# Performance work log

Hardware: AMD Instinct MI355X
Metric: run time of the kernel (lower is better)

The kernel has to match this reference:

```python
import jax, jax.numpy as jnp
import numpy as np

EPS = 1e-5

def layer_norm(x, g, b):
    m = jnp.mean(x, axis=-1, keepdims=True)
    v = jnp.mean((x - m) ** 2, axis=-1, keepdims=True)
    return (x - m) / jnp.sqrt(v + EPS) * g + b

def setup_inputs() -> dict:
    key = jax.random.key(0)
    ks = jax.random.split(key, 20)
    B, N, Fin, Fout, H, Fe = 8, 1024, 128, 128, 8, 16
    s = 0.02
    inp = {
        'x': jax.random.normal(ks[0], (B, N, Fin), jnp.float32),
        'adj': jax.random.randint(ks[1], (B, N, N), 0, 2, dtype=jnp.int32),
        'edge_attr': jax.random.normal(ks[2], (B, N, N, Fe), jnp.float32),
        'ln1_g': jnp.ones((Fin,), jnp.float32),
        'ln1_b': jnp.zeros((Fin,), jnp.float32),
        'Wp': s * jax.random.normal(ks[3], (Fout, Fin), jnp.float32),
        'bp': jnp.zeros((Fout,), jnp.float32),
        'eln_g': jnp.ones((Fe,), jnp.float32),
        'eln_b': jnp.zeros((Fe,), jnp.float32),
        'We1': s * jax.random.normal(ks[4], (2 * Fe, Fe), jnp.float32),
        'be1': jnp.zeros((2 * Fe,), jnp.float32),
        'We2': s * jax.random.normal(ks[5], (H, 2 * Fe), jnp.float32),
        'be2': jnp.zeros((H,), jnp.float32),
        'Wq': s * jax.random.normal(ks[6], (Fout, Fout), jnp.float32),
        'Wk': s * jax.random.normal(ks[7], (Fout, Fout), jnp.float32),
        'Wv': s * jax.random.normal(ks[8], (Fout, Fout), jnp.float32),
        'W1': s * jax.random.normal(ks[9], (2 * Fout, Fout), jnp.float32),
        'b1': jnp.zeros((2 * Fout,), jnp.float32),
        'W2': s * jax.random.normal(ks[10], (Fout, 2 * Fout), jnp.float32),
        'b2': jnp.zeros((Fout,), jnp.float32),
        'ln2_g': jnp.ones((Fout,), jnp.float32),
        'ln2_b': jnp.zeros((Fout,), jnp.float32),
    }
    return inp

def reference(x, adj, edge_attr, ln1_g, ln1_b, Wp, bp, eln_g, eln_b,
              We1, be1, We2, be2, Wq, Wk, Wv, W1, b1, W2, b2, ln2_g, ln2_b):
    B, N, _ = x.shape
    H = We2.shape[0]
    Fout = Wp.shape[0]
    Dh = Fout // H
    x_norm = layer_norm(x, ln1_g, ln1_b)
    x_proj = x_norm @ Wp.T + bp                       # [B,N,Fout]
    Q = (x_proj @ Wq.T).reshape(B, N, H, Dh).transpose(0, 2, 1, 3)  # [B,H,N,Dh]
    K = (x_proj @ Wk.T).reshape(B, N, H, Dh).transpose(0, 2, 1, 3)
    V = (x_proj @ Wv.T).reshape(B, N, H, Dh).transpose(0, 2, 1, 3)
    scores = jnp.einsum('bhnd,bhmd->bhnm', Q, K) / jnp.sqrt(jnp.float32(Dh))
    # edge bias MLP
    e = layer_norm(edge_attr, eln_g, eln_b)           # [B,N,N,Fe]
    e = jax.nn.relu(e @ We1.T + be1)
    edge_bias = (e @ We2.T + be2)                     # [B,N,N,H]
    scores = scores + edge_bias.transpose(0, 3, 1, 2)  # [B,H,N,N]
    scores = jnp.where(scores >= 0, scores, 0.2 * scores)  # LeakyReLU(0.2)
    mask = adj[:, None, :, :] != 0                    # [B,1,N,N]
    scores = jnp.where(mask, scores, jnp.float32(-1e9))
    probs = jax.nn.softmax(scores, axis=-1)
    context = jnp.einsum('bhnm,bhmd->bhnd', probs, V)  # [B,H,N,Dh]
    context = context.transpose(0, 2, 1, 3).reshape(B, N, Fout)
    h_attn = x_proj + context
    h = layer_norm(h_attn, ln2_g, ln2_b)
    h = jax.nn.relu(h @ W1.T + b1) @ W2.T + b2
    return h_attn + h
```

## Files before the change

kernel.cpp:

```cpp
#include <hip/hip_runtime.h>

#define LOG2E 1.44269504088896f

typedef __attribute__((ext_vector_type(8))) short bf8v;
typedef __attribute__((ext_vector_type(16))) float f16v;

union B8 { bf8v v; short s[8]; unsigned u[4]; uint2 d[2]; uint4 q; };
union F16 { f16v v; float f[16]; };

__device__ __forceinline__ unsigned short f2bf(float f) {
    union { float f; unsigned u; } c; c.f = f;
    unsigned r = c.u + 0x7FFFu + ((c.u >> 16) & 1u);
    return (unsigned short)(r >> 16);
}
__device__ __forceinline__ unsigned pk2(float a, float b) {
    return (unsigned)f2bf(a) | ((unsigned)f2bf(b) << 16);
}
__device__ __forceinline__ int rowpat(int reg, int half) {
    return (reg & 3) + 8 * (reg >> 2) + 4 * half;
}

__global__ __launch_bounds__(64) void ln_kernel(const float* __restrict__ x,
                                                const float* __restrict__ g,
                                                const float* __restrict__ b,
                                                float* __restrict__ y) {
    int row = blockIdx.x;
    int lane = threadIdx.x;
    const float* xr = x + (size_t)row * 128;
    float2 v = *(const float2*)(xr + lane * 2);
    float s = v.x + v.y;
    float sq = v.x * v.x + v.y * v.y;
    #pragma unroll
    for (int o = 32; o > 0; o >>= 1) { s += __shfl_xor(s, o); sq += __shfl_xor(sq, o); }
    float m = s * (1.f / 128.f);
    float var = sq * (1.f / 128.f) - m * m;
    float r = rsqrtf(fmaxf(var, 0.f) + 1e-5f);
    float2 gg = *(const float2*)(g + lane * 2);
    float2 bb = *(const float2*)(b + lane * 2);
    float2 o2;
    o2.x = (v.x - m) * r * gg.x + bb.x;
    o2.y = (v.y - m) * r * gg.y + bb.y;
    *(float2*)(y + (size_t)row * 128 + lane * 2) = o2;
}

__global__ __launch_bounds__(256) void gemm_kernel(const float* __restrict__ A,
                                                   const float* __restrict__ W,
                                                   const float* __restrict__ bias,
                                                   float* __restrict__ out,
                                                   const float* __restrict__ res,
                                                   int K, int ldo, int mode) {
    int t = threadIdx.x, w = t >> 6, lane = t & 63;
    int lm = lane & 31, half = lane >> 5;
    int row0 = blockIdx.x * 128 + w * 32;
    int col0 = blockIdx.y * 32;
    const float* ap = A + (size_t)(row0 + lm) * K + half * 8;
    const float* wp = W + (size_t)(col0 + lm) * K + half * 8;
    F16 acc;
    #pragma unroll
    for (int i = 0; i < 16; i++) acc.f[i] = 0.f;
    for (int k0 = 0; k0 < K; k0 += 16) {
        float4 a0 = *(const float4*)(ap + k0);
        float4 a1 = *(const float4*)(ap + k0 + 4);
        float4 w0 = *(const float4*)(wp + k0);
        float4 w1 = *(const float4*)(wp + k0 + 4);
        B8 af, wf;
        af.u[0] = pk2(a0.x, a0.y); af.u[1] = pk2(a0.z, a0.w);
        af.u[2] = pk2(a1.x, a1.y); af.u[3] = pk2(a1.z, a1.w);
        wf.u[0] = pk2(w0.x, w0.y); wf.u[1] = pk2(w0.z, w0.w);
        wf.u[2] = pk2(w1.x, w1.y); wf.u[3] = pk2(w1.z, w1.w);
        acc.v = __builtin_amdgcn_mfma_f32_32x32x16_bf16(af.v, wf.v, acc.v, 0, 0, 0);
    }
    float bv = bias ? bias[col0 + lm] : 0.f;
    int col = col0 + lm;
    #pragma unroll
    for (int reg = 0; reg < 16; reg++) {
        int row = row0 + rowpat(reg, half);
        float v = acc.f[reg] + bv;
        if (mode == 1) v = fmaxf(v, 0.f);
        if (mode == 2) v += res[(size_t)row * ldo + col];
        out[(size_t)row * ldo + col] = v;
    }
}

__global__ __launch_bounds__(512) void attn_kernel(
    const float* __restrict__ Qm, const float* __restrict__ Km, const float* __restrict__ Vm,
    const float* __restrict__ xp, const float* __restrict__ ea, const int* __restrict__ adj,
    const float* __restrict__ We1, const float* __restrict__ be1,
    const float* __restrict__ We2, const float* __restrict__ be2,
    const float* __restrict__ eg, const float* __restrict__ eb,
    float* __restrict__ ha) {
    __shared__ short smK[32][132];
    __shared__ short smVt[128][36];
    __shared__ float smBias[8480];
    __shared__ short smH1[8][1280];

    int b = blockIdx.x, i0 = blockIdx.y * 32;
    int t = threadIdx.x, w = t >> 6;
    int lane = t & 63, lm = lane & 31, half = lane >> 5;

    B8 qf, w1f, w2a, w2b;
    {
        const float* qp = Qm + (size_t)(b * 1024 + i0 + lm) * 128 + w * 16 + half * 8;
        float4 q0 = *(const float4*)qp, q1 = *(const float4*)(qp + 4);
        qf.u[0] = pk2(q0.x * 0.25f, q0.y * 0.25f); qf.u[1] = pk2(q0.z * 0.25f, q0.w * 0.25f);
        qf.u[2] = pk2(q1.x * 0.25f, q1.y * 0.25f); qf.u[3] = pk2(q1.z * 0.25f, q1.w * 0.25f);
    }
    {
        const float* wp = We1 + lm * 16 + half * 8;
        #pragma unroll
        for (int j = 0; j < 8; j++) w1f.s[j] = (short)f2bf(wp[j] * eg[half * 8 + j]);
    }
    {
        int hs = lm & 7;
        #pragma unroll
        for (int j = 0; j < 8; j++) {
            w2a.s[j] = (short)f2bf(We2[hs * 32 + half * 8 + j]);
            w2b.s[j] = (short)f2bf(We2[hs * 32 + 16 + half * 8 + j]);
        }
    }
    float c1r[16];
    #pragma unroll
    for (int reg = 0; reg < 16; reg++) {
        int ch = rowpat(reg, half);
        float sacc = be1[ch];
        const float* wr = We1 + ch * 16;
        #pragma unroll
        for (int j = 0; j < 16; j++) sacc += wr[j] * eb[j];
        c1r[reg] = sacc;
    }
    float be2r[4];
    #pragma unroll
    for (int r = 0; r < 4; r++) be2r[r] = be2[r + 4 * half];

    F16 ou;
    #pragma unroll
    for (int i = 0; i < 16; i++) ou.f[i] = 0.f;
    float mrun = -3.0e38f, lrun = 0.f;

    #pragma unroll 1
    for (int nj = 0; nj < 32; nj++) {
        int j0 = nj * 32;
        __syncthreads();
        {
            int rr = t >> 4, fc = (t & 15) * 8;
            const float* kp = Km + (size_t)(b * 1024 + j0 + rr) * 128 + fc;
            float4 k0 = *(const float4*)kp, k1 = *(const float4*)(kp + 4);
            uint2 p0; p0.x = pk2(k0.x, k0.y); p0.y = pk2(k0.z, k0.w);
            uint2 p1; p1.x = pk2(k1.x, k1.y); p1.y = pk2(k1.z, k1.w);
            *(uint2*)&smK[rr][fc] = p0;
            *(uint2*)&smK[rr][fc + 4] = p1;
            const float* vp = Vm + (size_t)(b * 1024 + j0 + rr) * 128 + fc;
            float4 v0 = *(const float4*)vp, v1 = *(const float4*)(vp + 4);
            smVt[fc + 0][rr] = (short)f2bf(v0.x); smVt[fc + 1][rr] = (short)f2bf(v0.y);
            smVt[fc + 2][rr] = (short)f2bf(v0.z); smVt[fc + 3][rr] = (short)f2bf(v0.w);
            smVt[fc + 4][rr] = (short)f2bf(v1.x); smVt[fc + 5][rr] = (short)f2bf(v1.y);
            smVt[fc + 6][rr] = (short)f2bf(v1.z); smVt[fc + 7][rr] = (short)f2bf(v1.w);
        }
        short* hrow = &smH1[w][lm * 40];
        for (int s4 = 0; s4 < 4; s4++) {
            int ti = w * 4 + s4;
            const float* ep = ea + ((size_t)(b * 1024 + i0 + ti) * 1024 + j0 + lm) * 16 + half * 8;
            float4 e0 = *(const float4*)ep, e1 = *(const float4*)(ep + 4);
            float sum = e0.x + e0.y + e0.z + e0.w + e1.x + e1.y + e1.z + e1.w;
            float sq = e0.x * e0.x + e0.y * e0.y + e0.z * e0.z + e0.w * e0.w
                     + e1.x * e1.x + e1.y * e1.y + e1.z * e1.z + e1.w * e1.w;
            sum += __shfl_xor(sum, 32); sq += __shfl_xor(sq, 32);
            float mn = sum * 0.0625f;
            float rs = rsqrtf(fmaxf(sq * 0.0625f - mn * mn, 0.f) + 1e-5f);
            float mr = mn * rs;
            B8 ef;
            ef.u[0] = pk2(e0.x * rs - mr, e0.y * rs - mr);
            ef.u[1] = pk2(e0.z * rs - mr, e0.w * rs - mr);
            ef.u[2] = pk2(e1.x * rs - mr, e1.y * rs - mr);
            ef.u[3] = pk2(e1.z * rs - mr, e1.w * rs - mr);
            F16 z;
            #pragma unroll
            for (int i = 0; i < 16; i++) z.f[i] = 0.f;
            F16 h1; h1.v = __builtin_amdgcn_mfma_f32_32x32x16_bf16(w1f.v, ef.v, z.v, 0, 0, 0);
            #pragma unroll
            for (int pr = 0; pr < 8; pr++) {
                int r0 = 2 * pr;
                int ch0 = rowpat(r0, half);
                float a0 = fmaxf(h1.f[r0] + c1r[r0], 0.f);
                float a1 = fmaxf(h1.f[r0 + 1] + c1r[r0 + 1], 0.f);
                *(unsigned*)(hrow + ch0) = pk2(a0, a1);
            }
            B8 hba, hbb;
            hba.q = *(const uint4*)(hrow + half * 8);
            hbb.q = *(const uint4*)(hrow + 16 + half * 8);
            F16 b2; b2.v = __builtin_amdgcn_mfma_f32_32x32x16_bf16(w2a.v, hba.v, z.v, 0, 0, 0);
            b2.v = __builtin_amdgcn_mfma_f32_32x32x16_bf16(w2b.v, hbb.v, b2.v, 0, 0, 0);
            int aj = adj[(size_t)(b * 1024 + i0 + ti) * 1024 + j0 + lm];
            #pragma unroll
            for (int reg = 0; reg < 4; reg++) {
                float bvv = aj ? (b2.f[reg] + be2r[reg]) : -1.0e9f;
                smBias[lm * 265 + (reg + 4 * half) * 33 + ti] = bvv;
            }
        }
        __syncthreads();
        F16 sc;
        #pragma unroll
        for (int reg = 0; reg < 16; reg++) {
            int tj = rowpat(reg, half);
            sc.f[reg] = smBias[tj * 265 + w * 33 + lm];
        }
        B8 kf;
        {
            const short* kp2 = &smK[lm][w * 16 + half * 8];
            kf.d[0] = *(const uint2*)kp2; kf.d[1] = *(const uint2*)(kp2 + 4);
        }
        F16 s; s.v = __builtin_amdgcn_mfma_f32_32x32x16_bf16(kf.v, qf.v, sc.v, 0, 0, 0);
        float mx = -3.0e38f;
        #pragma unroll
        for (int reg = 0; reg < 16; reg++) {
            float vv = s.f[reg];
            vv = fmaxf(vv, 0.2f * vv);
            s.f[reg] = vv;
            mx = fmaxf(mx, vv);
        }
        mx = fmaxf(mx, __shfl_xor(mx, 32));
        float mnew = fmaxf(mrun, mx);
        float al = exp2f((mrun - mnew) * LOG2E);
        float psum = 0.f;
        #pragma unroll
        for (int reg = 0; reg < 16; reg++) {
            float p = exp2f((s.f[reg] - mnew) * LOG2E);
            s.f[reg] = p; psum += p;
        }
        lrun = lrun * al + psum; mrun = mnew;
        unsigned q0 = pk2(s.f[0], s.f[1]), q0b = pk2(s.f[2], s.f[3]);
        unsigned q1 = pk2(s.f[4], s.f[5]), q1b = pk2(s.f[6], s.f[7]);
        unsigned q2 = pk2(s.f[8], s.f[9]), q2b = pk2(s.f[10], s.f[11]);
        unsigned q3 = pk2(s.f[12], s.f[13]), q3b = pk2(s.f[14], s.f[15]);
        unsigned x0 = __shfl_xor((int)q0, 32), x0b = __shfl_xor((int)q0b, 32);
        unsigned x1 = __shfl_xor((int)q1, 32), x1b = __shfl_xor((int)q1b, 32);
        unsigned x2 = __shfl_xor((int)q2, 32), x2b = __shfl_xor((int)q2b, 32);
        unsigned x3 = __shfl_xor((int)q3, 32), x3b = __shfl_xor((int)q3b, 32);
        B8 pfa, pfb;
        pfa.u[0] = half ? x1 : q0;  pfa.u[1] = half ? x1b : q0b;
        pfa.u[2] = half ? q1 : x0;  pfa.u[3] = half ? q1b : x0b;
        pfb.u[0] = half ? x3 : q2;  pfb.u[1] = half ? x3b : q2b;
        pfb.u[2] = half ? q3 : x2;  pfb.u[3] = half ? q3b : x2b;
        #pragma unroll
        for (int reg = 0; reg < 16; reg++) {
            float av = __shfl(al, rowpat(reg, half));
            ou.f[reg] *= av;
        }
        int dcol = lm & 15;
        const short* vp2 = &smVt[w * 16 + dcol][half * 8];
        B8 vfa, vfb;
        vfa.d[0] = *(const uint2*)vp2;        vfa.d[1] = *(const uint2*)(vp2 + 4);
        vfb.d[0] = *(const uint2*)(vp2 + 16); vfb.d[1] = *(const uint2*)(vp2 + 20);
        ou.v = __builtin_amdgcn_mfma_f32_32x32x16_bf16(pfa.v, vfa.v, ou.v, 0, 0, 0);
        ou.v = __builtin_amdgcn_mfma_f32_32x32x16_bf16(pfb.v, vfb.v, ou.v, 0, 0, 0);
    }
    float ltot = lrun + __shfl_xor(lrun, 32);
    float linv = 1.f / ltot;
    int dcol = lm & 15;
    #pragma unroll
    for (int reg = 0; reg < 16; reg++) {
        int row = rowpat(reg, half);
        float lv = __shfl(linv, row);
        if (lm < 16) {
            size_t gi = (size_t)(b * 1024 + i0 + row) * 128 + w * 16 + dcol;
            ha[gi] = ou.f[reg] * lv + xp[gi];
        }
    }
}

extern "C" void kernel_launch(void* const* d_in, const int* in_sizes, int n_in,
                              void* d_out, int out_size, void* d_ws, size_t ws_size,
                              hipStream_t stream) {
    (void)in_sizes; (void)n_in; (void)out_size; (void)ws_size;
    const float* x    = (const float*)d_in[0];
    const int*   adj  = (const int*)d_in[1];
    const float* ea   = (const float*)d_in[2];
    const float* ln1g = (const float*)d_in[3];
    const float* ln1b = (const float*)d_in[4];
    const float* Wp   = (const float*)d_in[5];
    const float* bp   = (const float*)d_in[6];
    const float* eg   = (const float*)d_in[7];
    const float* eb   = (const float*)d_in[8];
    const float* We1  = (const float*)d_in[9];
    const float* be1  = (const float*)d_in[10];
    const float* We2  = (const float*)d_in[11];
    const float* be2  = (const float*)d_in[12];
    const float* Wq   = (const float*)d_in[13];
    const float* Wk   = (const float*)d_in[14];
    const float* Wv   = (const float*)d_in[15];
    const float* W1   = (const float*)d_in[16];
    const float* b1   = (const float*)d_in[17];
    const float* W2   = (const float*)d_in[18];
    const float* b2   = (const float*)d_in[19];
    const float* ln2g = (const float*)d_in[20];
    const float* ln2b = (const float*)d_in[21];
    float* out = (float*)d_out;
    float* ws = (float*)d_ws;

    const size_t M1 = (size_t)8 * 1024 * 128;
    float* xn    = ws;
    float* xproj = ws + 1 * M1;
    float* Qb    = ws + 2 * M1;
    float* Kb    = ws + 3 * M1;
    float* Vb    = ws + 4 * M1;
    float* haw   = ws + 5 * M1;
    float* hn    = ws + 6 * M1;
    float* h1b   = ws + 7 * M1;

    ln_kernel<<<dim3(8192), dim3(64), 0, stream>>>(x, ln1g, ln1b, xn);
    gemm_kernel<<<dim3(64, 4), dim3(256), 0, stream>>>(xn, Wp, bp, xproj, nullptr, 128, 128, 0);
    gemm_kernel<<<dim3(64, 4), dim3(256), 0, stream>>>(xproj, Wq, nullptr, Qb, nullptr, 128, 128, 0);
    gemm_kernel<<<dim3(64, 4), dim3(256), 0, stream>>>(xproj, Wk, nullptr, Kb, nullptr, 128, 128, 0);
    gemm_kernel<<<dim3(64, 4), dim3(256), 0, stream>>>(xproj, Wv, nullptr, Vb, nullptr, 128, 128, 0);
    attn_kernel<<<dim3(8, 32), dim3(512), 0, stream>>>(Qb, Kb, Vb, xproj, ea, adj,
                                                       We1, be1, We2, be2, eg, eb, haw);
    ln_kernel<<<dim3(8192), dim3(64), 0, stream>>>(haw, ln2g, ln2b, hn);
    gemm_kernel<<<dim3(64, 8), dim3(256), 0, stream>>>(hn, W1, b1, h1b, nullptr, 128, 256, 1);
    gemm_kernel<<<dim3(64, 4), dim3(256), 0, stream>>>(h1b, W2, b2, out, haw, 256, 128, 2);
}
```

Baseline: 937.8 us.

## Split attention over key halves, use bf16 intermediates and register-shuffle edge MLP

Attention now runs on a 3D grid that splits the key range into two halves, giving twice as many blocks on the GPU, with a new combine kernel that merges the partial softmax results (max and sum) and adds the residual. All intermediates and weights between GEMMs are stored as bf16 (weights are pre-converted, and the Q scale is folded into Wq), so GEMM and attention loads need no conversion. The edge MLP replaces the LDS round-trip with cross-lane shuffles and folds the biases into the MFMA accumulator inputs. pk2 uses a hardware pack-convert builtin when one exists. The costs are an extra pass and buffer traffic for the partial outputs, plus the weight conversion run on every call.

```diff
diff --git a/kernel.cpp b/kernel.cpp
--- a/kernel.cpp
+++ b/kernel.cpp
@@ -2,6 +2,7 @@
 
 #define LOG2E 1.44269504088896f
 
+typedef unsigned short u16;
 typedef __attribute__((ext_vector_type(8))) short bf8v;
 typedef __attribute__((ext_vector_type(16))) float f16v;
 
@@ -14,16 +15,37 @@
     return (unsigned short)(r >> 16);
 }
 __device__ __forceinline__ unsigned pk2(float a, float b) {
+#if __has_builtin(__builtin_amdgcn_cvt_pk_bf16_f32)
+    typedef __attribute__((ext_vector_type(2))) __bf16 vbf2;
+    union { vbf2 v; unsigned u; } c;
+    c.v = __builtin_amdgcn_cvt_pk_bf16_f32(a, b);
+    return c.u;
+#else
     return (unsigned)f2bf(a) | ((unsigned)f2bf(b) << 16);
-}
+#endif
+}
+__device__ __forceinline__ u16 f2bf1(float a) { return (u16)(pk2(a, a) & 0xffffu); }
 __device__ __forceinline__ int rowpat(int reg, int half) {
     return (reg & 3) + 8 * (reg >> 2) + 4 * half;
 }
 
-__global__ __launch_bounds__(64) void ln_kernel(const float* __restrict__ x,
-                                                const float* __restrict__ g,
-                                                const float* __restrict__ b,
-                                                float* __restrict__ y) {
+__global__ __launch_bounds__(256) void cvtw_kernel(const float* __restrict__ w0, const float* __restrict__ w1,
+                                                   const float* __restrict__ w2, const float* __restrict__ w3,
+                                                   const float* __restrict__ w4, const float* __restrict__ w5,
+                                                   u16* __restrict__ o) {
+    const int sizes[6] = {16384, 16384, 16384, 16384, 32768, 32768};
+    const int offs[6]  = {0, 16384, 32768, 49152, 65536, 98304};
+    int y = blockIdx.y;
+    int idx = blockIdx.x * 256 + threadIdx.x;
+    const float* src = y == 0 ? w0 : y == 1 ? w1 : y == 2 ? w2 : y == 3 ? w3 : y == 4 ? w4 : w5;
+    float scale = (y == 1) ? 0.25f : 1.0f;
+    if (idx < sizes[y]) o[offs[y] + idx] = f2bf1(src[idx] * scale);
+}
+
+__global__ __launch_bounds__(64) void ln_bf16_kernel(const float* __restrict__ x,
+                                                     const float* __restrict__ g,
+                                                     const float* __restrict__ b,
+                                                     u16* __restrict__ y) {
     int row = blockIdx.x;
     int lane = threadIdx.x;
     const float* xr = x + (size_t)row * 128;
@@ -37,74 +59,61 @@
     float r = rsqrtf(fmaxf(var, 0.f) + 1e-5f);
     float2 gg = *(const float2*)(g + lane * 2);
     float2 bb = *(const float2*)(b + lane * 2);
-    float2 o2;
-    o2.x = (v.x - m) * r * gg.x + bb.x;
-    o2.y = (v.y - m) * r * gg.y + bb.y;
-    *(float2*)(y + (size_t)row * 128 + lane * 2) = o2;
-}
-
-__global__ __launch_bounds__(256) void gemm_kernel(const float* __restrict__ A,
-                                                   const float* __restrict__ W,
-                                                   const float* __restrict__ bias,
-                                                   float* __restrict__ out,
-                                                   const float* __restrict__ res,
-                                                   int K, int ldo, int mode) {
+    unsigned p = pk2((v.x - m) * r * gg.x + bb.x, (v.y - m) * r * gg.y + bb.y);
+    *(unsigned*)(y + (size_t)row * 128 + lane * 2) = p;
+}
+
+template<int K, int MODE>
+__global__ __launch_bounds__(256) void gemm_bb(const u16* __restrict__ A, const u16* __restrict__ W,
+                                               const float* __restrict__ bias,
+                                               float* __restrict__ outf, u16* __restrict__ outb,
+                                               const float* __restrict__ res, int ldo) {
     int t = threadIdx.x, w = t >> 6, lane = t & 63;
     int lm = lane & 31, half = lane >> 5;
     int row0 = blockIdx.x * 128 + w * 32;
     int col0 = blockIdx.y * 32;
-    const float* ap = A + (size_t)(row0 + lm) * K + half * 8;
-    const float* wp = W + (size_t)(col0 + lm) * K + half * 8;
+    const u16* ap = A + (size_t)(row0 + lm) * K + half * 8;
+    const u16* wp = W + (size_t)(col0 + lm) * K + half * 8;
     F16 acc;
     #pragma unroll
     for (int i = 0; i < 16; i++) acc.f[i] = 0.f;
+    #pragma unroll
     for (int k0 = 0; k0 < K; k0 += 16) {
-        float4 a0 = *(const float4*)(ap + k0);
-        float4 a1 = *(const float4*)(ap + k0 + 4);
-        float4 w0 = *(const float4*)(wp + k0);
-        float4 w1 = *(const float4*)(wp + k0 + 4);
         B8 af, wf;
-        af.u[0] = pk2(a0.x, a0.y); af.u[1] = pk2(a0.z, a0.w);
-        af.u[2] = pk2(a1.x, a1.y); af.u[3] = pk2(a1.z, a1.w);
-        wf.u[0] = pk2(w0.x, w0.y); wf.u[1] = pk2(w0.z, w0.w);
-        wf.u[2] = pk2(w1.x, w1.y); wf.u[3] = pk2(w1.z, w1.w);
+        af.q = *(const uint4*)(ap + k0);
+        wf.q = *(const uint4*)(wp + k0);
         acc.v = __builtin_amdgcn_mfma_f32_32x32x16_bf16(af.v, wf.v, acc.v, 0, 0, 0);
     }
-    float bv = bias ? bias[col0 + lm] : 0.f;
     int col = col0 + lm;
+    float bv = (MODE != 0) ? bias[col] : 0.f;
     #pragma unroll
     for (int reg = 0; reg < 16; reg++) {
         int row = row0 + rowpat(reg, half);
         float v = acc.f[reg] + bv;
-        if (mode == 1) v = fmaxf(v, 0.f);
-        if (mode == 2) v += res[(size_t)row * ldo + col];
-        out[(size_t)row * ldo + col] = v;
-    }
-}
-
-__global__ __launch_bounds__(512) void attn_kernel(
-    const float* __restrict__ Qm, const float* __restrict__ Km, const float* __restrict__ Vm,
-    const float* __restrict__ xp, const float* __restrict__ ea, const int* __restrict__ adj,
+        if (MODE == 0) outb[(size_t)row * ldo + col] = f2bf1(v);
+        if (MODE == 1) outb[(size_t)row * ldo + col] = f2bf1(fmaxf(v, 0.f));
+        if (MODE == 2) outf[(size_t)row * ldo + col] = v + res[(size_t)row * ldo + col];
+        if (MODE == 3) { outf[(size_t)row * ldo + col] = v; outb[(size_t)row * ldo + col] = f2bf1(v); }
+    }
+}
+
+__global__ __launch_bounds__(512, 4) void attn_kernel(
+    const u16* __restrict__ Qm, const u16* __restrict__ Km, const u16* __restrict__ Vm,
+    const float* __restrict__ ea, const int* __restrict__ adj,
     const float* __restrict__ We1, const float* __restrict__ be1,
     const float* __restrict__ We2, const float* __restrict__ be2,
     const float* __restrict__ eg, const float* __restrict__ eb,
-    float* __restrict__ ha) {
-    __shared__ short smK[32][132];
-    __shared__ short smVt[128][36];
+    float* __restrict__ Opart, float* __restrict__ ml) {
+    __shared__ u16 smK[32][132];
+    __shared__ u16 smVt[128][36];
     __shared__ float smBias[8480];
-    __shared__ short smH1[8][1280];
-
-    int b = blockIdx.x, i0 = blockIdx.y * 32;
+
+    int b = blockIdx.x, i0 = blockIdx.y * 32, z = blockIdx.z;
     int t = threadIdx.x, w = t >> 6;
     int lane = t & 63, lm = lane & 31, half = lane >> 5;
 
     B8 qf, w1f, w2a, w2b;
-    {
-        const float* qp = Qm + (size_t)(b * 1024 + i0 + lm) * 128 + w * 16 + half * 8;
-        float4 q0 = *(const float4*)qp, q1 = *(const float4*)(qp + 4);
-        qf.u[0] = pk2(q0.x * 0.25f, q0.y * 0.25f); qf.u[1] = pk2(q0.z * 0.25f, q0.w * 0.25f);
-        qf.u[2] = pk2(q1.x * 0.25f, q1.y * 0.25f); qf.u[3] = pk2(q1.z * 0.25f, q1.w * 0.25f);
-    }
+    qf.q = *(const uint4*)(Qm + (size_t)(b * 1024 + i0 + lm) * 128 + w * 16 + half * 8);
     {
         const float* wp = We1 + lm * 16 + half * 8;
         #pragma unroll
@@ -118,7 +127,7 @@
             w2b.s[j] = (short)f2bf(We2[hs * 32 + 16 + half * 8 + j]);
         }
     }
-    float c1r[16];
+    F16 c1s;
     #pragma unroll
     for (int reg = 0; reg < 16; reg++) {
         int ch = rowpat(reg, half);
@@ -126,11 +135,13 @@
         const float* wr = We1 + ch * 16;
         #pragma unroll
         for (int j = 0; j < 16; j++) sacc += wr[j] * eb[j];
-        c1r[reg] = sacc;
-    }
-    float be2r[4];
-    #pragma unroll
-    for (int r = 0; r < 4; r++) be2r[r] = be2[r + 4 * half];
+        c1s.f[reg] = sacc;
+    }
+    F16 c2s;
+    #pragma unroll
+    for (int i = 0; i < 16; i++) c2s.f[i] = 0.f;
+    #pragma unroll
+    for (int r = 0; r < 4; r++) c2s.f[r] = be2[r + 4 * half];
 
     F16 ou;
     #pragma unroll
@@ -138,25 +149,22 @@
     float mrun = -3.0e38f, lrun = 0.f;
 
     #pragma unroll 1
-    for (int nj = 0; nj < 32; nj++) {
+    for (int nj = z * 16; nj < z * 16 + 16; nj++) {
         int j0 = nj * 32;
         __syncthreads();
         {
             int rr = t >> 4, fc = (t & 15) * 8;
-            const float* kp = Km + (size_t)(b * 1024 + j0 + rr) * 128 + fc;
-            float4 k0 = *(const float4*)kp, k1 = *(const float4*)(kp + 4);
-            uint2 p0; p0.x = pk2(k0.x, k0.y); p0.y = pk2(k0.z, k0.w);
-            uint2 p1; p1.x = pk2(k1.x, k1.y); p1.y = pk2(k1.z, k1.w);
-            *(uint2*)&smK[rr][fc] = p0;
-            *(uint2*)&smK[rr][fc + 4] = p1;
-            const float* vp = Vm + (size_t)(b * 1024 + j0 + rr) * 128 + fc;
-            float4 v0 = *(const float4*)vp, v1 = *(const float4*)(vp + 4);
-            smVt[fc + 0][rr] = (short)f2bf(v0.x); smVt[fc + 1][rr] = (short)f2bf(v0.y);
-            smVt[fc + 2][rr] = (short)f2bf(v0.z); smVt[fc + 3][rr] = (short)f2bf(v0.w);
-            smVt[fc + 4][rr] = (short)f2bf(v1.x); smVt[fc + 5][rr] = (short)f2bf(v1.y);
-            smVt[fc + 6][rr] = (short)f2bf(v1.z); smVt[fc + 7][rr] = (short)f2bf(v1.w);
-        }
-        short* hrow = &smH1[w][lm * 40];
+            uint4 kq = *(const uint4*)(Km + (size_t)(b * 1024 + j0 + rr) * 128 + fc);
+            uint2 ka; ka.x = kq.x; ka.y = kq.y;
+            uint2 kb; kb.x = kq.z; kb.y = kq.w;
+            *(uint2*)&smK[rr][fc] = ka;
+            *(uint2*)&smK[rr][fc + 4] = kb;
+            uint4 vq = *(const uint4*)(Vm + (size_t)(b * 1024 + j0 + rr) * 128 + fc);
+            smVt[fc + 0][rr] = (u16)(vq.x & 0xffffu); smVt[fc + 1][rr] = (u16)(vq.x >> 16);
+            smVt[fc + 2][rr] = (u16)(vq.y & 0xffffu); smVt[fc + 3][rr] = (u16)(vq.y >> 16);
+            smVt[fc + 4][rr] = (u16)(vq.z & 0xffffu); smVt[fc + 5][rr] = (u16)(vq.z >> 16);
+            smVt[fc + 6][rr] = (u16)(vq.w & 0xffffu); smVt[fc + 7][rr] = (u16)(vq.w >> 16);
+        }
         for (int s4 = 0; s4 < 4; s4++) {
             int ti = w * 4 + s4;
             const float* ep = ea + ((size_t)(b * 1024 + i0 + ti) * 1024 + j0 + lm) * 16 + half * 8;
@@ -173,27 +181,30 @@
             ef.u[1] = pk2(e0.z * rs - mr, e0.w * rs - mr);
             ef.u[2] = pk2(e1.x * rs - mr, e1.y * rs - mr);
             ef.u[3] = pk2(e1.z * rs - mr, e1.w * rs - mr);
-            F16 z;
-            #pragma unroll
-            for (int i = 0; i < 16; i++) z.f[i] = 0.f;
-            F16 h1; h1.v = __builtin_amdgcn_mfma_f32_32x32x16_bf16(w1f.v, ef.v, z.v, 0, 0, 0);
-            #pragma unroll
-            for (int pr = 0; pr < 8; pr++) {
-                int r0 = 2 * pr;
-                int ch0 = rowpat(r0, half);
-                float a0 = fmaxf(h1.f[r0] + c1r[r0], 0.f);
-                float a1 = fmaxf(h1.f[r0 + 1] + c1r[r0 + 1], 0.f);
-                *(unsigned*)(hrow + ch0) = pk2(a0, a1);
-            }
+            F16 h1; h1.v = __builtin_amdgcn_mfma_f32_32x32x16_bf16(w1f.v, ef.v, c1s.v, 0, 0, 0);
+            unsigned a01 = pk2(fmaxf(h1.f[0], 0.f),  fmaxf(h1.f[1], 0.f));
+            unsigned a23 = pk2(fmaxf(h1.f[2], 0.f),  fmaxf(h1.f[3], 0.f));
+            unsigned a45 = pk2(fmaxf(h1.f[4], 0.f),  fmaxf(h1.f[5], 0.f));
+            unsigned a67 = pk2(fmaxf(h1.f[6], 0.f),  fmaxf(h1.f[7], 0.f));
+            unsigned a89 = pk2(fmaxf(h1.f[8], 0.f),  fmaxf(h1.f[9], 0.f));
+            unsigned aAB = pk2(fmaxf(h1.f[10], 0.f), fmaxf(h1.f[11], 0.f));
+            unsigned aCD = pk2(fmaxf(h1.f[12], 0.f), fmaxf(h1.f[13], 0.f));
+            unsigned aEF = pk2(fmaxf(h1.f[14], 0.f), fmaxf(h1.f[15], 0.f));
+            unsigned x01 = __shfl_xor((int)a01, 32), x23 = __shfl_xor((int)a23, 32);
+            unsigned x45 = __shfl_xor((int)a45, 32), x67 = __shfl_xor((int)a67, 32);
+            unsigned x89 = __shfl_xor((int)a89, 32), xAB = __shfl_xor((int)aAB, 32);
+            unsigned xCD = __shfl_xor((int)aCD, 32), xEF = __shfl_xor((int)aEF, 32);
             B8 hba, hbb;
-            hba.q = *(const uint4*)(hrow + half * 8);
-            hbb.q = *(const uint4*)(hrow + 16 + half * 8);
-            F16 b2; b2.v = __builtin_amdgcn_mfma_f32_32x32x16_bf16(w2a.v, hba.v, z.v, 0, 0, 0);
+            hba.u[0] = half ? x45 : a01;  hba.u[1] = half ? x67 : a23;
+            hba.u[2] = half ? a45 : x01;  hba.u[3] = half ? a67 : x23;
+            hbb.u[0] = half ? xCD : a89;  hbb.u[1] = half ? xEF : aAB;
+            hbb.u[2] = half ? aCD : x89;  hbb.u[3] = half ? aEF : xAB;
+            F16 b2; b2.v = __builtin_amdgcn_mfma_f32_32x32x16_bf16(w2a.v, hba.v, c2s.v, 0, 0, 0);
             b2.v = __builtin_amdgcn_mfma_f32_32x32x16_bf16(w2b.v, hbb.v, b2.v, 0, 0, 0);
             int aj = adj[(size_t)(b * 1024 + i0 + ti) * 1024 + j0 + lm];
             #pragma unroll
             for (int reg = 0; reg < 4; reg++) {
-                float bvv = aj ? (b2.f[reg] + be2r[reg]) : -1.0e9f;
+                float bvv = aj ? b2.f[reg] : -1.0e9f;
                 smBias[lm * 265 + (reg + 4 * half) * 33 + ti] = bvv;
             }
         }
@@ -206,7 +217,7 @@
         }
         B8 kf;
         {
-            const short* kp2 = &smK[lm][w * 16 + half * 8];
+            const u16* kp2 = &smK[lm][w * 16 + half * 8];
             kf.d[0] = *(const uint2*)kp2; kf.d[1] = *(const uint2*)(kp2 + 4);
         }
         F16 s; s.v = __builtin_amdgcn_mfma_f32_32x32x16_bf16(kf.v, qf.v, sc.v, 0, 0, 0);
@@ -228,9 +239,9 @@
             s.f[reg] = p; psum += p;
         }
         lrun = lrun * al + psum; mrun = mnew;
-        unsigned q0 = pk2(s.f[0], s.f[1]), q0b = pk2(s.f[2], s.f[3]);
-        unsigned q1 = pk2(s.f[4], s.f[5]), q1b = pk2(s.f[6], s.f[7]);
-        unsigned q2 = pk2(s.f[8], s.f[9]), q2b = pk2(s.f[10], s.f[11]);
+        unsigned q0 = pk2(s.f[0], s.f[1]),   q0b = pk2(s.f[2], s.f[3]);
+        unsigned q1 = pk2(s.f[4], s.f[5]),   q1b = pk2(s.f[6], s.f[7]);
+        unsigned q2 = pk2(s.f[8], s.f[9]),   q2b = pk2(s.f[10], s.f[11]);
         unsigned q3 = pk2(s.f[12], s.f[13]), q3b = pk2(s.f[14], s.f[15]);
         unsigned x0 = __shfl_xor((int)q0, 32), x0b = __shfl_xor((int)q0b, 32);
         unsigned x1 = __shfl_xor((int)q1, 32), x1b = __shfl_xor((int)q1b, 32);
@@ -247,7 +258,7 @@
             ou.f[reg] *= av;
         }
         int dcol = lm & 15;
-        const short* vp2 = &smVt[w * 16 + dcol][half * 8];
+        const u16* vp2 = &smVt[w * 16 + dcol][half * 8];
         B8 vfa, vfb;
         vfa.d[0] = *(const uint2*)vp2;        vfa.d[1] = *(const uint2*)(vp2 + 4);
         vfb.d[0] = *(const uint2*)(vp2 + 16); vfb.d[1] = *(const uint2*)(vp2 + 20);
@@ -255,17 +266,37 @@
         ou.v = __builtin_amdgcn_mfma_f32_32x32x16_bf16(pfb.v, vfb.v, ou.v, 0, 0, 0);
     }
     float ltot = lrun + __shfl_xor(lrun, 32);
-    float linv = 1.f / ltot;
+    if (half == 0) {
+        size_t mli = (((size_t)z * 8192 + b * 1024 + i0 + lm) * 8 + w) * 2;
+        ml[mli] = mrun; ml[mli + 1] = ltot;
+    }
     int dcol = lm & 15;
     #pragma unroll
     for (int reg = 0; reg < 16; reg++) {
         int row = rowpat(reg, half);
-        float lv = __shfl(linv, row);
         if (lm < 16) {
-            size_t gi = (size_t)(b * 1024 + i0 + row) * 128 + w * 16 + dcol;
-            ha[gi] = ou.f[reg] * lv + xp[gi];
-        }
-    }
+            Opart[((size_t)z * 8192 + b * 1024 + i0 + row) * 128 + w * 16 + dcol] = ou.f[reg];
+        }
+    }
+}
+
+__global__ __launch_bounds__(256) void combine_kernel(const float* __restrict__ O,
+                                                      const float* __restrict__ ml,
+                                                      const float* __restrict__ xp,
+                                                      float* __restrict__ haw) {
+    int t = threadIdx.x;
+    int row = blockIdx.x * 2 + (t >> 7);
+    int f = t & 127;
+    int h = f >> 4;
+    size_t base = (size_t)row * 128 + f;
+    const float* mlp = ml + ((size_t)row * 8 + h) * 2;
+    float m1 = mlp[0], l1 = mlp[1];
+    float m2 = mlp[(size_t)8192 * 16], l2 = mlp[(size_t)8192 * 16 + 1];
+    float m = fmaxf(m1, m2);
+    float a1 = exp2f((m1 - m) * LOG2E), a2 = exp2f((m2 - m) * LOG2E);
+    float l = l1 * a1 + l2 * a2;
+    float o = O[base] * a1 + O[(size_t)8192 * 128 + base] * a2;
+    haw[base] = o / l + xp[base];
 }
 
 extern "C" void kernel_launch(void* const* d_in, const int* in_sizes, int n_in,
@@ -295,26 +326,31 @@
     const float* ln2g = (const float*)d_in[20];
     const float* ln2b = (const float*)d_in[21];
     float* out = (float*)d_out;
-    float* ws = (float*)d_ws;
-
-    const size_t M1 = (size_t)8 * 1024 * 128;
-    float* xn    = ws;
-    float* xproj = ws + 1 * M1;
-    float* Qb    = ws + 2 * M1;
-    float* Kb    = ws + 3 * M1;
-    float* Vb    = ws + 4 * M1;
-    float* haw   = ws + 5 * M1;
-    float* hn    = ws + 6 * M1;
-    float* h1b   = ws + 7 * M1;
-
-    ln_kernel<<<dim3(8192), dim3(64), 0, stream>>>(x, ln1g, ln1b, xn);
-    gemm_kernel<<<dim3(64, 4), dim3(256), 0, stream>>>(xn, Wp, bp, xproj, nullptr, 128, 128, 0);
-    gemm_kernel<<<dim3(64, 4), dim3(256), 0, stream>>>(xproj, Wq, nullptr, Qb, nullptr, 128, 128, 0);
-    gemm_kernel<<<dim3(64, 4), dim3(256), 0, stream>>>(xproj, Wk, nullptr, Kb, nullptr, 128, 128, 0);
-    gemm_kernel<<<dim3(64, 4), dim3(256), 0, stream>>>(xproj, Wv, nullptr, Vb, nullptr, 128, 128, 0);
-    attn_kernel<<<dim3(8, 32), dim3(512), 0, stream>>>(Qb, Kb, Vb, xproj, ea, adj,
-                                                       We1, be1, We2, be2, eg, eb, haw);
-    ln_kernel<<<dim3(8192), dim3(64), 0, stream>>>(haw, ln2g, ln2b, hn);
-    gemm_kernel<<<dim3(64, 8), dim3(256), 0, stream>>>(hn, W1, b1, h1b, nullptr, 128, 256, 1);
-    gemm_kernel<<<dim3(64, 4), dim3(256), 0, stream>>>(h1b, W2, b2, out, haw, 256, 128, 2);
-}
+    char* wsb = (char*)d_ws;
+
+    float* xprojF = (float*)(wsb);
+    float* haw    = (float*)(wsb + ((size_t)4  << 20));
+    float* Opart  = (float*)(wsb + ((size_t)8  << 20));
+    float* mlbuf  = (float*)(wsb + ((size_t)16 << 20));
+    u16*   xnB    = (u16*)  (wsb + ((size_t)17 << 20));
+    u16*   xprojB = (u16*)  (wsb + ((size_t)19 << 20));
+    u16*   Qb     = (u16*)  (wsb + ((size_t)21 << 20));
+    u16*   Kb     = (u16*)  (wsb + ((size_t)23 << 20));
+    u16*   Vb     = (u16*)  (wsb + ((size_t)25 << 20));
+    u16*   hnB    = (u16*)  (wsb + ((size_t)27 << 20));
+    u16*   h1bB   = (u16*)  (wsb + ((size_t)29 << 20));
+    u16*   WB     = (u16*)  (wsb + ((size_t)33 << 20));
+
+    cvtw_kernel<<<dim3(128, 6), dim3(256), 0, stream>>>(Wp, Wq, Wk, Wv, W1, W2, WB);
+    ln_bf16_kernel<<<dim3(8192), dim3(64), 0, stream>>>(x, ln1g, ln1b, xnB);
+    gemm_bb<128, 3><<<dim3(64, 4), dim3(256), 0, stream>>>(xnB, WB, bp, xprojF, xprojB, nullptr, 128);
+    gemm_bb<128, 0><<<dim3(64, 4), dim3(256), 0, stream>>>(xprojB, WB + 16384, nullptr, nullptr, Qb, nullptr, 128);
+    gemm_bb<128, 0><<<dim3(64, 4), dim3(256), 0, stream>>>(xprojB, WB + 32768, nullptr, nullptr, Kb, nullptr, 128);
+    gemm_bb<128, 0><<<dim3(64, 4), dim3(256), 0, stream>>>(xprojB, WB + 49152, nullptr, nullptr, Vb, nullptr, 128);
+    attn_kernel<<<dim3(8, 32, 2), dim3(512), 0, stream>>>(Qb, Kb, Vb, ea, adj,
+                                                          We1, be1, We2, be2, eg, eb, Opart, mlbuf);
+    combine_kernel<<<dim3(4096), dim3(256), 0, stream>>>(Opart, mlbuf, xprojF, haw);
+    ln_bf16_kernel<<<dim3(8192), dim3(64), 0, stream>>>(haw, ln2g, ln2b, hnB);
+    gemm_bb<128, 1><<<dim3(64, 8), dim3(256), 0, stream>>>(hnB, WB + 65536, b1, nullptr, h1bB, nullptr, 256);
+    gemm_bb<256, 2><<<dim3(64, 4), dim3(256), 0, stream>>>(h1bB, WB + 98304, b2, out, nullptr, haw, 128);
+}
```

Result: faster. 860.4 us (-8.3%).
